# Optimization experiments

Measured on AMD Instinct MI355X. Metric: run time of the kernel, lower is better.

## Reference

```python
import jax, jax.numpy as jnp
import numpy as np

INV_SQRT2 = 0.7071067811865476  # Haar/db1 filter coefficient
LEVEL = 3


def _split(x, axis):
    """One Haar analysis step along `axis` (even length assumed)."""
    ax = axis % x.ndim
    sl0 = [slice(None)] * x.ndim; sl0[ax] = slice(0, None, 2)
    sl1 = [slice(None)] * x.ndim; sl1[ax] = slice(1, None, 2)
    x0, x1 = x[tuple(sl0)], x[tuple(sl1)]
    return (x0 + x1) * INV_SQRT2, (x0 - x1) * INV_SQRT2


def _merge(lo, hi, axis):
    """One Haar synthesis step along `axis` (interleave even/odd)."""
    ax = axis % lo.ndim
    e = (lo + hi) * INV_SQRT2
    o = (lo - hi) * INV_SQRT2
    s = jnp.stack([e, o], axis=ax + 1)
    shape = list(lo.shape)
    shape[ax] *= 2
    return s.reshape(shape)


def _dwt2(x):
    lo, hi = _split(x, -1)
    a, h = _split(lo, -2)
    v, d = _split(hi, -2)
    return a, h, v, d


def _idwt2(a, h, v, d):
    lo = _merge(a, h, -2)
    hi = _merge(v, d, -2)
    return _merge(lo, hi, -1)


def setup_inputs() -> dict:
    key = jax.random.key(0)
    ks = jax.random.split(key, 8)
    B, H, W = 16, 1024, 1024
    x = jax.random.normal(ks[0], (B, H, W, 1), dtype=jnp.float32)
    na = (H // 8) * (W // 8)   # approx size at level 3
    n2 = (H // 4) * (W // 4)
    n1 = (H // 2) * (W // 2)
    scale = 0.02
    Wa = jax.random.normal(ks[1], (na, 1), dtype=jnp.float32) * scale
    ba = jnp.zeros((1,), jnp.float32)
    Wd1 = jax.random.normal(ks[2], (3 * na, 3), dtype=jnp.float32) * scale  # coarsest details
    bd1 = jnp.zeros((3,), jnp.float32)
    Wd2 = jax.random.normal(ks[3], (3 * n2, 3), dtype=jnp.float32) * scale
    bd2 = jnp.zeros((3,), jnp.float32)
    Wd3 = jax.random.normal(ks[4], (3 * n1, 3), dtype=jnp.float32) * scale  # finest details
    bd3 = jnp.zeros((3,), jnp.float32)
    return {"x": x, "Wa": Wa, "ba": ba, "Wd1": Wd1, "bd1": bd1,
            "Wd2": Wd2, "bd2": bd2, "Wd3": Wd3, "bd3": bd3}


def reference(x, Wa, ba, Wd1, bd1, Wd2, bd2, Wd3, bd3):
    img = x[..., 0]                      # [B, H, W]
    B = img.shape[0]
    details = []                         # finest -> coarsest
    cur = img
    for _ in range(LEVEL):
        cur, h, v, d = _dwt2(cur)
        details.append((h, v, d))
    # approximation attention: sigmoid(Dense(1)) scalar gate per sample
    aw = jax.nn.sigmoid(cur.reshape(B, -1) @ Wa + ba)   # [B, 1]
    rec = cur * aw[:, :, None]                           # [B, H/8, W/8]
    # detail attention per level (coarsest first, matching pywt coeff order)
    det_params = [(Wd1, bd1), (Wd2, bd2), (Wd3, bd3)]
    for (h, v, d), (Wd, bd) in zip(reversed(details), det_params):
        flat = jnp.stack([h, v, d], axis=1).reshape(B, -1)      # [B, 3*hl*wl]
        w = jax.nn.softmax(flat @ Wd + bd, axis=-1)             # [B, 3]
        rec = _idwt2(rec,
                     h * w[:, 0, None, None],
                     v * w[:, 1, None, None],
                     d * w[:, 2, None, None])
    return rec                                                   # [B, H, W]
```

## Files before the change

### kernel.cpp

```cpp
#include <hip/hip_runtime.h>
#include <math.h>

#define HH 1024
#define WW 1024
#define N1 262144
#define N2 65536
#define N3 16384
#define BLOCKS_PER_B 64

#define C_INV_SQRT2 0.70710678118654752440f

static __device__ __forceinline__ void haar_fwd(float P, float Q, float R, float S,
                                                float& a, float& h, float& v, float& d) {
    const float C = C_INV_SQRT2;
    float lo0 = (P + Q) * C, lo1 = (R + S) * C;
    float hi0 = (P - Q) * C, hi1 = (R - S) * C;
    a = (lo0 + lo1) * C; h = (lo0 - lo1) * C;
    v = (hi0 + hi1) * C; d = (hi0 - hi1) * C;
}

static __device__ __forceinline__ void haar_inv(float a, float h, float v, float d,
                                                float& P, float& Q, float& R, float& S) {
    const float C = C_INV_SQRT2;
    float elo = (a + h) * C, olo = (a - h) * C;
    float ehi = (v + d) * C, ohi = (v - d) * C;
    P = (elo + ehi) * C; Q = (elo - ehi) * C;
    R = (olo + ohi) * C; S = (olo - ohi) * C;
}

__global__ __launch_bounds__(256) void wa_fwd_dots(
    const float* __restrict__ x,
    const float* __restrict__ Wa,
    const float* __restrict__ Wd1,
    const float* __restrict__ Wd2,
    const float* __restrict__ Wd3,
    float* __restrict__ partial)
{
    const int b = blockIdx.z;
    const int t = threadIdx.x;
    const int tr = t >> 4, tc = t & 15;
    const int y0 = blockIdx.y * 128 + tr * 8;
    const int x0 = blockIdx.x * 128 + tc * 8;

    const float* xb = x + (size_t)b * HH * WW;

    float p[8][8];
    #pragma unroll
    for (int r = 0; r < 8; ++r) {
        const float4* row = (const float4*)(xb + (size_t)(y0 + r) * WW + x0);
        float4 u0 = row[0], u1 = row[1];
        p[r][0] = u0.x; p[r][1] = u0.y; p[r][2] = u0.z; p[r][3] = u0.w;
        p[r][4] = u1.x; p[r][5] = u1.y; p[r][6] = u1.z; p[r][7] = u1.w;
    }

    float acc[10];
    #pragma unroll
    for (int k = 0; k < 10; ++k) acc[k] = 0.f;

    float a1[4][4];
    #pragma unroll
    for (int i = 0; i < 4; ++i) {
        const size_t jj0 = (size_t)((y0 >> 1) + i) * 512 + (size_t)(x0 >> 1);
        float wh[12], wv[12], wd[12];
        {
            const float4* H = (const float4*)(Wd3 + jj0 * 3);
            const float4* V = (const float4*)(Wd3 + (jj0 + (size_t)N1) * 3);
            const float4* D = (const float4*)(Wd3 + (jj0 + (size_t)2 * N1) * 3);
            #pragma unroll
            for (int q = 0; q < 3; ++q) {
                float4 a = H[q]; wh[4*q] = a.x; wh[4*q+1] = a.y; wh[4*q+2] = a.z; wh[4*q+3] = a.w;
                float4 c = V[q]; wv[4*q] = c.x; wv[4*q+1] = c.y; wv[4*q+2] = c.z; wv[4*q+3] = c.w;
                float4 e = D[q]; wd[4*q] = e.x; wd[4*q+1] = e.y; wd[4*q+2] = e.z; wd[4*q+3] = e.w;
            }
        }
        #pragma unroll
        for (int j = 0; j < 4; ++j) {
            float a, h, v, d;
            haar_fwd(p[2*i][2*j], p[2*i][2*j+1], p[2*i+1][2*j], p[2*i+1][2*j+1], a, h, v, d);
            a1[i][j] = a;
            #pragma unroll
            for (int c = 0; c < 3; ++c)
                acc[7 + c] += h * wh[j*3 + c] + v * wv[j*3 + c] + d * wd[j*3 + c];
        }
    }

    float a2[2][2];
    #pragma unroll
    for (int i = 0; i < 2; ++i) {
        const size_t jj0 = (size_t)((y0 >> 2) + i) * 256 + (size_t)(x0 >> 2);
        float wh[6], wv[6], wd[6];
        {
            const float2* H = (const float2*)(Wd2 + jj0 * 3);
            const float2* V = (const float2*)(Wd2 + (jj0 + (size_t)N2) * 3);
            const float2* D = (const float2*)(Wd2 + (jj0 + (size_t)2 * N2) * 3);
            #pragma unroll
            for (int q = 0; q < 3; ++q) {
                float2 a = H[q]; wh[2*q] = a.x; wh[2*q+1] = a.y;
                float2 c = V[q]; wv[2*q] = c.x; wv[2*q+1] = c.y;
                float2 e = D[q]; wd[2*q] = e.x; wd[2*q+1] = e.y;
            }
        }
        #pragma unroll
        for (int j = 0; j < 2; ++j) {
            float a, h, v, d;
            haar_fwd(a1[2*i][2*j], a1[2*i][2*j+1], a1[2*i+1][2*j], a1[2*i+1][2*j+1], a, h, v, d);
            a2[i][j] = a;
            #pragma unroll
            for (int c = 0; c < 3; ++c)
                acc[4 + c] += h * wh[j*3 + c] + v * wv[j*3 + c] + d * wd[j*3 + c];
        }
    }

    {
        float a, h, v, d;
        haar_fwd(a2[0][0], a2[0][1], a2[1][0], a2[1][1], a, h, v, d);
        const size_t jj = (size_t)(y0 >> 3) * 128 + (size_t)(x0 >> 3);
        acc[0] += a * Wa[jj];
        const float* wh = Wd1 + jj * 3;
        const float* wv = Wd1 + (jj + (size_t)N3) * 3;
        const float* wd = Wd1 + (jj + (size_t)2 * N3) * 3;
        #pragma unroll
        for (int c = 0; c < 3; ++c)
            acc[1 + c] += h * wh[c] + v * wv[c] + d * wd[c];
    }

    #pragma unroll
    for (int k = 0; k < 10; ++k) {
        float s = acc[k];
        #pragma unroll
        for (int off = 32; off > 0; off >>= 1) s += __shfl_down(s, off, 64);
        acc[k] = s;
    }
    __shared__ float red[4][10];
    const int lane = t & 63, wave = t >> 6;
    if (lane == 0) {
        #pragma unroll
        for (int k = 0; k < 10; ++k) red[wave][k] = acc[k];
    }
    __syncthreads();
    if (t < 10) {
        const int blkflat = b * BLOCKS_PER_B + blockIdx.y * 8 + blockIdx.x;
        partial[(size_t)blkflat * 10 + t] = red[0][t] + red[1][t] + red[2][t] + red[3][t];
    }
}

__global__ __launch_bounds__(64) void wa_gates(
    const float* __restrict__ partial,
    const float* __restrict__ ba,
    const float* __restrict__ bd1,
    const float* __restrict__ bd2,
    const float* __restrict__ bd3,
    float* __restrict__ gates)
{
    const int b = blockIdx.x;
    const int l = threadIdx.x;
    const float* row = partial + (size_t)(b * BLOCKS_PER_B + l) * 10;
    float v[10];
    #pragma unroll
    for (int k = 0; k < 10; ++k) v[k] = row[k];
    #pragma unroll
    for (int k = 0; k < 10; ++k) {
        #pragma unroll
        for (int off = 32; off > 0; off >>= 1) v[k] += __shfl_down(v[k], off, 64);
    }
    if (l == 0) {
        float* G = gates + b * 10;
        G[0] = 1.f / (1.f + expf(-(v[0] + ba[0])));
        const float* bds[3] = { bd1, bd2, bd3 };
        #pragma unroll
        for (int lv = 0; lv < 3; ++lv) {
            float l0 = v[1 + 3*lv + 0] + bds[lv][0];
            float l1 = v[1 + 3*lv + 1] + bds[lv][1];
            float l2 = v[1 + 3*lv + 2] + bds[lv][2];
            float m = fmaxf(l0, fmaxf(l1, l2));
            float e0 = expf(l0 - m), e1 = expf(l1 - m), e2 = expf(l2 - m);
            float inv = 1.f / (e0 + e1 + e2);
            G[1 + 3*lv + 0] = e0 * inv;
            G[1 + 3*lv + 1] = e1 * inv;
            G[1 + 3*lv + 2] = e2 * inv;
        }
    }
}

__global__ __launch_bounds__(64) void wa_recon(
    const float* __restrict__ x,
    const float* __restrict__ gates,
    float* __restrict__ out)
{
    const int b = blockIdx.z;
    const int t = threadIdx.x;

    __shared__ float g[10];
    if (t < 10) g[t] = gates[b * 10 + t];
    __syncthreads();

    const int tr = t >> 3, tc = t & 7;
    const int y0 = blockIdx.y * 64 + tr * 8;
    const int x0 = blockIdx.x * 64 + tc * 8;

    const float* xb = x + (size_t)b * HH * WW;

    float p[8][8];
    #pragma unroll
    for (int r = 0; r < 8; ++r) {
        const float4* row = (const float4*)(xb + (size_t)(y0 + r) * WW + x0);
        float4 u0 = row[0], u1 = row[1];
        p[r][0] = u0.x; p[r][1] = u0.y; p[r][2] = u0.z; p[r][3] = u0.w;
        p[r][4] = u1.x; p[r][5] = u1.y; p[r][6] = u1.z; p[r][7] = u1.w;
    }

    float a1[4][4], h1[4][4], v1[4][4], d1[4][4];
    #pragma unroll
    for (int i = 0; i < 4; ++i)
        #pragma unroll
        for (int j = 0; j < 4; ++j)
            haar_fwd(p[2*i][2*j], p[2*i][2*j+1], p[2*i+1][2*j], p[2*i+1][2*j+1],
                     a1[i][j], h1[i][j], v1[i][j], d1[i][j]);

    float a2[2][2], h2[2][2], v2[2][2], d2[2][2];
    #pragma unroll
    for (int i = 0; i < 2; ++i)
        #pragma unroll
        for (int j = 0; j < 2; ++j)
            haar_fwd(a1[2*i][2*j], a1[2*i][2*j+1], a1[2*i+1][2*j], a1[2*i+1][2*j+1],
                     a2[i][j], h2[i][j], v2[i][j], d2[i][j]);

    float a3, h3, v3, d3;
    haar_fwd(a2[0][0], a2[0][1], a2[1][0], a2[1][1], a3, h3, v3, d3);

    a3 *= g[0];
    float r2[2][2];
    haar_inv(a3, h3 * g[1], v3 * g[2], d3 * g[3],
             r2[0][0], r2[0][1], r2[1][0], r2[1][1]);

    float r1[4][4];
    #pragma unroll
    for (int i = 0; i < 2; ++i)
        #pragma unroll
        for (int j = 0; j < 2; ++j)
            haar_inv(r2[i][j], h2[i][j] * g[4], v2[i][j] * g[5], d2[i][j] * g[6],
                     r1[2*i][2*j], r1[2*i][2*j+1], r1[2*i+1][2*j], r1[2*i+1][2*j+1]);

    float r0[8][8];
    #pragma unroll
    for (int i = 0; i < 4; ++i)
        #pragma unroll
        for (int j = 0; j < 4; ++j)
            haar_inv(r1[i][j], h1[i][j] * g[7], v1[i][j] * g[8], d1[i][j] * g[9],
                     r0[2*i][2*j], r0[2*i][2*j+1], r0[2*i+1][2*j], r0[2*i+1][2*j+1]);

    float* ob = out + (size_t)b * HH * WW;
    #pragma unroll
    for (int r = 0; r < 8; ++r) {
        float4* row = (float4*)(ob + (size_t)(y0 + r) * WW + x0);
        float4 u0, u1;
        u0.x = r0[r][0]; u0.y = r0[r][1]; u0.z = r0[r][2]; u0.w = r0[r][3];
        u1.x = r0[r][4]; u1.y = r0[r][5]; u1.z = r0[r][6]; u1.w = r0[r][7];
        row[0] = u0; row[1] = u1;
    }
}

extern "C" void kernel_launch(void* const* d_in, const int* in_sizes, int n_in,
                              void* d_out, int out_size, void* d_ws, size_t ws_size,
                              hipStream_t stream) {
    const float* x   = (const float*)d_in[0];
    const float* Wa  = (const float*)d_in[1];
    const float* ba  = (const float*)d_in[2];
    const float* Wd1 = (const float*)d_in[3];
    const float* bd1 = (const float*)d_in[4];
    const float* Wd2 = (const float*)d_in[5];
    const float* bd2 = (const float*)d_in[6];
    const float* Wd3 = (const float*)d_in[7];
    const float* bd3 = (const float*)d_in[8];
    float* out = (float*)d_out;

    const int B = in_sizes[0] / (HH * WW);

    float* partial = (float*)d_ws;
    float* gates   = partial + (size_t)B * BLOCKS_PER_B * 10;

    dim3 fgrid(8, 8, B);
    wa_fwd_dots<<<fgrid, 256, 0, stream>>>(x, Wa, Wd1, Wd2, Wd3, partial);
    wa_gates<<<B, 64, 0, stream>>>(partial, ba, bd1, bd2, bd3, gates);
    dim3 rgrid(16, 16, B);
    wa_recon<<<rgrid, 64, 0, stream>>>(x, gates, out);
}
```

Before: 172.7 us.

## Split 8x8 Haar tiles across four lanes with shuffle exchange for coarser levels

Each thread now loads a 2x8 strip instead of an 8x8 block, and groups of four lanes cooperate on one 8x8 tile, exchanging level-1 and level-2 approximation coefficients via __shfl_xor. Blocks cover 512x8 strips, so each wave reads full contiguous rows for coalescing, and register pressure drops, which allows higher occupancy (launch_bounds 256,8). The gate kernel now sums more per-block partials in a loop. The cost is extra shuffles and select logic, plus some idle lanes at the coarser levels.

```diff
diff --git a/kernel.cpp b/kernel.cpp
--- a/kernel.cpp
+++ b/kernel.cpp
@@ -6,7 +6,8 @@
 #define N1 262144
 #define N2 65536
 #define N3 16384
-#define BLOCKS_PER_B 64
+#define TILE_W 512
+#define BLOCKS_PER_B ((WW / TILE_W) * (HH / 8))
 
 #define C_INV_SQRT2 0.70710678118654752440f
 
@@ -28,7 +29,7 @@
     R = (olo + ohi) * C; S = (olo - ohi) * C;
 }
 
-__global__ __launch_bounds__(256) void wa_fwd_dots(
+__global__ __launch_bounds__(256, 8) void wa_fwd_dots(
     const float* __restrict__ x,
     const float* __restrict__ Wa,
     const float* __restrict__ Wd1,
@@ -38,15 +39,16 @@
 {
     const int b = blockIdx.z;
     const int t = threadIdx.x;
-    const int tr = t >> 4, tc = t & 15;
-    const int y0 = blockIdx.y * 128 + tr * 8;
-    const int x0 = blockIdx.x * 128 + tc * 8;
+    const int k = t >> 2;
+    const int q = t & 3;
+    const int x0 = blockIdx.x * TILE_W + k * 8;
+    const int y0 = blockIdx.y * 8 + q * 2;
 
     const float* xb = x + (size_t)b * HH * WW;
 
-    float p[8][8];
-    #pragma unroll
-    for (int r = 0; r < 8; ++r) {
+    float p[2][8];
+    #pragma unroll
+    for (int r = 0; r < 2; ++r) {
         const float4* row = (const float4*)(xb + (size_t)(y0 + r) * WW + x0);
         float4 u0 = row[0], u1 = row[1];
         p[r][0] = u0.x; p[r][1] = u0.y; p[r][2] = u0.z; p[r][3] = u0.w;
@@ -55,66 +57,84 @@
 
     float acc[10];
     #pragma unroll
-    for (int k = 0; k < 10; ++k) acc[k] = 0.f;
-
-    float a1[4][4];
-    #pragma unroll
-    for (int i = 0; i < 4; ++i) {
-        const size_t jj0 = (size_t)((y0 >> 1) + i) * 512 + (size_t)(x0 >> 1);
-        float wh[12], wv[12], wd[12];
-        {
-            const float4* H = (const float4*)(Wd3 + jj0 * 3);
-            const float4* V = (const float4*)(Wd3 + (jj0 + (size_t)N1) * 3);
-            const float4* D = (const float4*)(Wd3 + (jj0 + (size_t)2 * N1) * 3);
+    for (int c = 0; c < 10; ++c) acc[c] = 0.f;
+
+    float a1[4], hh[4], vv[4], dd[4];
+    #pragma unroll
+    for (int j = 0; j < 4; ++j)
+        haar_fwd(p[0][2*j], p[0][2*j+1], p[1][2*j], p[1][2*j+1],
+                 a1[j], hh[j], vv[j], dd[j]);
+    {
+        const size_t jj0 = (size_t)(blockIdx.y * 4 + q) * 512 + (size_t)(x0 >> 1);
+        const float4* H = (const float4*)(Wd3 + jj0 * 3);
+        const float4* V = (const float4*)(Wd3 + (jj0 + (size_t)N1) * 3);
+        const float4* D = (const float4*)(Wd3 + (jj0 + (size_t)2 * N1) * 3);
+        #pragma unroll
+        for (int s = 0; s < 3; ++s) {
+            const float4* W4 = (s == 0) ? H : (s == 1) ? V : D;
+            const float*  cf = (s == 0) ? hh : (s == 1) ? vv : dd;
+            float w[12];
             #pragma unroll
-            for (int q = 0; q < 3; ++q) {
-                float4 a = H[q]; wh[4*q] = a.x; wh[4*q+1] = a.y; wh[4*q+2] = a.z; wh[4*q+3] = a.w;
-                float4 c = V[q]; wv[4*q] = c.x; wv[4*q+1] = c.y; wv[4*q+2] = c.z; wv[4*q+3] = c.w;
-                float4 e = D[q]; wd[4*q] = e.x; wd[4*q+1] = e.y; wd[4*q+2] = e.z; wd[4*q+3] = e.w;
+            for (int u = 0; u < 3; ++u) {
+                float4 f = W4[u];
+                w[4*u] = f.x; w[4*u+1] = f.y; w[4*u+2] = f.z; w[4*u+3] = f.w;
             }
+            #pragma unroll
+            for (int j = 0; j < 4; ++j)
+                #pragma unroll
+                for (int c = 0; c < 3; ++c)
+                    acc[7 + c] += cf[j] * w[3*j + c];
         }
-        #pragma unroll
-        for (int j = 0; j < 4; ++j) {
-            float a, h, v, d;
-            haar_fwd(p[2*i][2*j], p[2*i][2*j+1], p[2*i+1][2*j], p[2*i+1][2*j+1], a, h, v, d);
-            a1[i][j] = a;
+    }
+
+    float o1[4];
+    #pragma unroll
+    for (int j = 0; j < 4; ++j) o1[j] = __shfl_xor(a1[j], 1);
+    const bool odd = (q & 1);
+    float top[4], bot[4];
+    #pragma unroll
+    for (int j = 0; j < 4; ++j) {
+        top[j] = odd ? o1[j] : a1[j];
+        bot[j] = odd ? a1[j] : o1[j];
+    }
+    float a2[2], h2[2], v2[2], d2[2];
+    #pragma unroll
+    for (int j = 0; j < 2; ++j)
+        haar_fwd(top[2*j], top[2*j+1], bot[2*j], bot[2*j+1],
+                 a2[j], h2[j], v2[j], d2[j]);
+    if (!odd) {
+        const size_t kk0 = (size_t)(blockIdx.y * 2 + (q >> 1)) * 256 + (size_t)(x0 >> 2);
+        const float2* H = (const float2*)(Wd2 + kk0 * 3);
+        const float2* V = (const float2*)(Wd2 + (kk0 + (size_t)N2) * 3);
+        const float2* D = (const float2*)(Wd2 + (kk0 + (size_t)2 * N2) * 3);
+        float wh[6], wv[6], wd[6];
+        #pragma unroll
+        for (int u = 0; u < 3; ++u) {
+            float2 fh = H[u]; wh[2*u] = fh.x; wh[2*u+1] = fh.y;
+            float2 fv = V[u]; wv[2*u] = fv.x; wv[2*u+1] = fv.y;
+            float2 fd = D[u]; wd[2*u] = fd.x; wd[2*u+1] = fd.y;
+        }
+        #pragma unroll
+        for (int j = 0; j < 2; ++j)
             #pragma unroll
             for (int c = 0; c < 3; ++c)
-                acc[7 + c] += h * wh[j*3 + c] + v * wv[j*3 + c] + d * wd[j*3 + c];
-        }
-    }
-
-    float a2[2][2];
-    #pragma unroll
-    for (int i = 0; i < 2; ++i) {
-        const size_t jj0 = (size_t)((y0 >> 2) + i) * 256 + (size_t)(x0 >> 2);
-        float wh[6], wv[6], wd[6];
-        {
-            const float2* H = (const float2*)(Wd2 + jj0 * 3);
-            const float2* V = (const float2*)(Wd2 + (jj0 + (size_t)N2) * 3);
-            const float2* D = (const float2*)(Wd2 + (jj0 + (size_t)2 * N2) * 3);
-            #pragma unroll
-            for (int q = 0; q < 3; ++q) {
-                float2 a = H[q]; wh[2*q] = a.x; wh[2*q+1] = a.y;
-                float2 c = V[q]; wv[2*q] = c.x; wv[2*q+1] = c.y;
-                float2 e = D[q]; wd[2*q] = e.x; wd[2*q+1] = e.y;
-            }
-        }
-        #pragma unroll
-        for (int j = 0; j < 2; ++j) {
-            float a, h, v, d;
-            haar_fwd(a1[2*i][2*j], a1[2*i][2*j+1], a1[2*i+1][2*j], a1[2*i+1][2*j+1], a, h, v, d);
-            a2[i][j] = a;
-            #pragma unroll
-            for (int c = 0; c < 3; ++c)
-                acc[4 + c] += h * wh[j*3 + c] + v * wv[j*3 + c] + d * wd[j*3 + c];
-        }
-    }
-
-    {
+                acc[4 + c] += h2[j] * wh[3*j + c] + v2[j] * wv[3*j + c] + d2[j] * wd[3*j + c];
+    }
+
+    float o2[2];
+    #pragma unroll
+    for (int j = 0; j < 2; ++j) o2[j] = __shfl_xor(a2[j], 2);
+    const bool lower = (q >> 1);
+    float t3[2], b3[2];
+    #pragma unroll
+    for (int j = 0; j < 2; ++j) {
+        t3[j] = lower ? o2[j] : a2[j];
+        b3[j] = lower ? a2[j] : o2[j];
+    }
+    if (q == 0) {
         float a, h, v, d;
-        haar_fwd(a2[0][0], a2[0][1], a2[1][0], a2[1][1], a, h, v, d);
-        const size_t jj = (size_t)(y0 >> 3) * 128 + (size_t)(x0 >> 3);
+        haar_fwd(t3[0], t3[1], b3[0], b3[1], a, h, v, d);
+        const size_t jj = (size_t)blockIdx.y * 128 + (size_t)(x0 >> 3);
         acc[0] += a * Wa[jj];
         const float* wh = Wd1 + jj * 3;
         const float* wv = Wd1 + (jj + (size_t)N3) * 3;
@@ -125,21 +145,21 @@
     }
 
     #pragma unroll
-    for (int k = 0; k < 10; ++k) {
-        float s = acc[k];
+    for (int c = 0; c < 10; ++c) {
+        float s = acc[c];
         #pragma unroll
         for (int off = 32; off > 0; off >>= 1) s += __shfl_down(s, off, 64);
-        acc[k] = s;
+        acc[c] = s;
     }
     __shared__ float red[4][10];
     const int lane = t & 63, wave = t >> 6;
     if (lane == 0) {
         #pragma unroll
-        for (int k = 0; k < 10; ++k) red[wave][k] = acc[k];
+        for (int c = 0; c < 10; ++c) red[wave][c] = acc[c];
     }
     __syncthreads();
     if (t < 10) {
-        const int blkflat = b * BLOCKS_PER_B + blockIdx.y * 8 + blockIdx.x;
+        const int blkflat = b * BLOCKS_PER_B + blockIdx.y * (WW / TILE_W) + blockIdx.x;
         partial[(size_t)blkflat * 10 + t] = red[0][t] + red[1][t] + red[2][t] + red[3][t];
     }
 }
@@ -154,14 +174,19 @@
 {
     const int b = blockIdx.x;
     const int l = threadIdx.x;
-    const float* row = partial + (size_t)(b * BLOCKS_PER_B + l) * 10;
     float v[10];
     #pragma unroll
-    for (int k = 0; k < 10; ++k) v[k] = row[k];
-    #pragma unroll
-    for (int k = 0; k < 10; ++k) {
-        #pragma unroll
-        for (int off = 32; off > 0; off >>= 1) v[k] += __shfl_down(v[k], off, 64);
+    for (int c = 0; c < 10; ++c) v[c] = 0.f;
+    #pragma unroll
+    for (int rep = 0; rep < BLOCKS_PER_B / 64; ++rep) {
+        const float* row = partial + (size_t)(b * BLOCKS_PER_B + rep * 64 + l) * 10;
+        #pragma unroll
+        for (int c = 0; c < 10; ++c) v[c] += row[c];
+    }
+    #pragma unroll
+    for (int c = 0; c < 10; ++c) {
+        #pragma unroll
+        for (int off = 32; off > 0; off >>= 1) v[c] += __shfl_down(v[c], off, 64);
     }
     if (l == 0) {
         float* G = gates + b * 10;
@@ -182,7 +207,7 @@
     }
 }
 
-__global__ __launch_bounds__(64) void wa_recon(
+__global__ __launch_bounds__(256, 8) void wa_recon(
     const float* __restrict__ x,
     const float* __restrict__ gates,
     float* __restrict__ out)
@@ -194,64 +219,85 @@
     if (t < 10) g[t] = gates[b * 10 + t];
     __syncthreads();
 
-    const int tr = t >> 3, tc = t & 7;
-    const int y0 = blockIdx.y * 64 + tr * 8;
-    const int x0 = blockIdx.x * 64 + tc * 8;
+    const int k = t >> 2;
+    const int q = t & 3;
+    const int x0 = blockIdx.x * TILE_W + k * 8;
+    const int y0 = blockIdx.y * 8 + q * 2;
 
     const float* xb = x + (size_t)b * HH * WW;
 
-    float p[8][8];
-    #pragma unroll
-    for (int r = 0; r < 8; ++r) {
+    float p[2][8];
+    #pragma unroll
+    for (int r = 0; r < 2; ++r) {
         const float4* row = (const float4*)(xb + (size_t)(y0 + r) * WW + x0);
         float4 u0 = row[0], u1 = row[1];
         p[r][0] = u0.x; p[r][1] = u0.y; p[r][2] = u0.z; p[r][3] = u0.w;
         p[r][4] = u1.x; p[r][5] = u1.y; p[r][6] = u1.z; p[r][7] = u1.w;
     }
 
-    float a1[4][4], h1[4][4], v1[4][4], d1[4][4];
-    #pragma unroll
-    for (int i = 0; i < 4; ++i)
-        #pragma unroll
-        for (int j = 0; j < 4; ++j)
-            haar_fwd(p[2*i][2*j], p[2*i][2*j+1], p[2*i+1][2*j], p[2*i+1][2*j+1],
-                     a1[i][j], h1[i][j], v1[i][j], d1[i][j]);
-
-    float a2[2][2], h2[2][2], v2[2][2], d2[2][2];
-    #pragma unroll
-    for (int i = 0; i < 2; ++i)
-        #pragma unroll
-        for (int j = 0; j < 2; ++j)
-            haar_fwd(a1[2*i][2*j], a1[2*i][2*j+1], a1[2*i+1][2*j], a1[2*i+1][2*j+1],
-                     a2[i][j], h2[i][j], v2[i][j], d2[i][j]);
-
+    float a1[4], h1[4], v1[4], d1[4];
+    #pragma unroll
+    for (int j = 0; j < 4; ++j)
+        haar_fwd(p[0][2*j], p[0][2*j+1], p[1][2*j], p[1][2*j+1],
+                 a1[j], h1[j], v1[j], d1[j]);
+
+    float o1[4];
+    #pragma unroll
+    for (int j = 0; j < 4; ++j) o1[j] = __shfl_xor(a1[j], 1);
+    const bool odd = (q & 1);
+    float top[4], bot[4];
+    #pragma unroll
+    for (int j = 0; j < 4; ++j) {
+        top[j] = odd ? o1[j] : a1[j];
+        bot[j] = odd ? a1[j] : o1[j];
+    }
+    float a2[2], h2[2], v2[2], d2[2];
+    #pragma unroll
+    for (int j = 0; j < 2; ++j)
+        haar_fwd(top[2*j], top[2*j+1], bot[2*j], bot[2*j+1],
+                 a2[j], h2[j], v2[j], d2[j]);
+
+    float o2[2];
+    #pragma unroll
+    for (int j = 0; j < 2; ++j) o2[j] = __shfl_xor(a2[j], 2);
+    const bool lower = (q >> 1);
+    float t3[2], b3[2];
+    #pragma unroll
+    for (int j = 0; j < 2; ++j) {
+        t3[j] = lower ? o2[j] : a2[j];
+        b3[j] = lower ? a2[j] : o2[j];
+    }
     float a3, h3, v3, d3;
-    haar_fwd(a2[0][0], a2[0][1], a2[1][0], a2[1][1], a3, h3, v3, d3);
+    haar_fwd(t3[0], t3[1], b3[0], b3[1], a3, h3, v3, d3);
 
     a3 *= g[0];
     float r2[2][2];
     haar_inv(a3, h3 * g[1], v3 * g[2], d3 * g[3],
              r2[0][0], r2[0][1], r2[1][0], r2[1][1]);
-
-    float r1[4][4];
-    #pragma unroll
-    for (int i = 0; i < 2; ++i)
-        #pragma unroll
-        for (int j = 0; j < 2; ++j)
-            haar_inv(r2[i][j], h2[i][j] * g[4], v2[i][j] * g[5], d2[i][j] * g[6],
-                     r1[2*i][2*j], r1[2*i][2*j+1], r1[2*i+1][2*j], r1[2*i+1][2*j+1]);
-
-    float r0[8][8];
-    #pragma unroll
-    for (int i = 0; i < 4; ++i)
-        #pragma unroll
-        for (int j = 0; j < 4; ++j)
-            haar_inv(r1[i][j], h1[i][j] * g[7], v1[i][j] * g[8], d1[i][j] * g[9],
-                     r0[2*i][2*j], r0[2*i][2*j+1], r0[2*i+1][2*j], r0[2*i+1][2*j+1]);
+    const int i2 = q >> 1;
+    float r2m0 = r2[i2][0], r2m1 = r2[i2][1];
+
+    float r1[4];
+    {
+        float P, Q, R, S;
+        haar_inv(r2m0, h2[0] * g[4], v2[0] * g[5], d2[0] * g[6], P, Q, R, S);
+        r1[0] = odd ? R : P;  r1[1] = odd ? S : Q;
+        haar_inv(r2m1, h2[1] * g[4], v2[1] * g[5], d2[1] * g[6], P, Q, R, S);
+        r1[2] = odd ? R : P;  r1[3] = odd ? S : Q;
+    }
+
+    float r0[2][8];
+    #pragma unroll
+    for (int j = 0; j < 4; ++j) {
+        float P, Q, R, S;
+        haar_inv(r1[j], h1[j] * g[7], v1[j] * g[8], d1[j] * g[9], P, Q, R, S);
+        r0[0][2*j] = P; r0[0][2*j+1] = Q;
+        r0[1][2*j] = R; r0[1][2*j+1] = S;
+    }
 
     float* ob = out + (size_t)b * HH * WW;
     #pragma unroll
-    for (int r = 0; r < 8; ++r) {
+    for (int r = 0; r < 2; ++r) {
         float4* row = (float4*)(ob + (size_t)(y0 + r) * WW + x0);
         float4 u0, u1;
         u0.x = r0[r][0]; u0.y = r0[r][1]; u0.z = r0[r][2]; u0.w = r0[r][3];
@@ -279,9 +325,8 @@
     float* partial = (float*)d_ws;
     float* gates   = partial + (size_t)B * BLOCKS_PER_B * 10;
 
-    dim3 fgrid(8, 8, B);
-    wa_fwd_dots<<<fgrid, 256, 0, stream>>>(x, Wa, Wd1, Wd2, Wd3, partial);
+    dim3 grid(WW / TILE_W, HH / 8, B);
+    wa_fwd_dots<<<grid, 256, 0, stream>>>(x, Wa, Wd1, Wd2, Wd3, partial);
     wa_gates<<<B, 64, 0, stream>>>(partial, ba, bd1, bd2, bd3, gates);
-    dim3 rgrid(16, 16, B);
-    wa_recon<<<rgrid, 64, 0, stream>>>(x, gates, out);
-}
+    wa_recon<<<grid, 256, 0, stream>>>(x, gates, out);
+}
```

Measured after the change: 182.3 us. +5.6%, slower.

## Restructure DWT kernels into row strips with weights reused across batch images

Applied to the files above, without the earlier changes.

The forward-dot kernel now gives each block an 8-row strip and loops over a chunk of batch images. Each thread loads its weight slices into registers once and reuses them for every image in the chunk, which cuts repeated weight reads from global memory. Each thread now owns a 4-wide column pair, and the level-3 step combines values from neighbouring lanes with shuffles. The reconstruction kernel uses the same strip layout with 256-thread blocks. Per-wave partial sums are written to a larger partial buffer that the gate kernel reduces with a strided loop. The trade-off is more register pressure from the cached weights and fewer blocks in the forward grid.

```diff
diff --git a/kernel.cpp b/kernel.cpp
--- a/kernel.cpp
+++ b/kernel.cpp
@@ -6,7 +6,8 @@
 #define N1 262144
 #define N2 65536
 #define N3 16384
-#define BLOCKS_PER_B 64
+#define NCHUNK 4
+#define ROWS_PER_IMG 512
 
 #define C_INV_SQRT2 0.70710678118654752440f
 
@@ -34,113 +35,110 @@
     const float* __restrict__ Wd1,
     const float* __restrict__ Wd2,
     const float* __restrict__ Wd3,
-    float* __restrict__ partial)
+    float* __restrict__ partial,
+    int ipc)
 {
-    const int b = blockIdx.z;
+    const int strip = blockIdx.x;
+    const int chunk = blockIdx.y;
     const int t = threadIdx.x;
-    const int tr = t >> 4, tc = t & 15;
-    const int y0 = blockIdx.y * 128 + tr * 8;
-    const int x0 = blockIdx.x * 128 + tc * 8;
-
-    const float* xb = x + (size_t)b * HH * WW;
-
-    float p[8][8];
-    #pragma unroll
-    for (int r = 0; r < 8; ++r) {
-        const float4* row = (const float4*)(xb + (size_t)(y0 + r) * WW + x0);
-        float4 u0 = row[0], u1 = row[1];
-        p[r][0] = u0.x; p[r][1] = u0.y; p[r][2] = u0.z; p[r][3] = u0.w;
-        p[r][4] = u1.x; p[r][5] = u1.y; p[r][6] = u1.z; p[r][7] = u1.w;
-    }
-
-    float acc[10];
-    #pragma unroll
-    for (int k = 0; k < 10; ++k) acc[k] = 0.f;
-
-    float a1[4][4];
-    #pragma unroll
-    for (int i = 0; i < 4; ++i) {
-        const size_t jj0 = (size_t)((y0 >> 1) + i) * 512 + (size_t)(x0 >> 1);
-        float wh[12], wv[12], wd[12];
+    const int lane = t & 63, wave = t >> 6;
+
+    float w1[3][4][6];
+    #pragma unroll
+    for (int qr = 0; qr < 4; ++qr) {
+        const size_t jj = (size_t)(strip * 4 + qr) * 512 + 2 * t;
+        #pragma unroll
+        for (int s = 0; s < 3; ++s) {
+            const float2* src = (const float2*)(Wd3 + (jj + (size_t)s * N1) * 3);
+            float2 f0 = src[0], f1 = src[1], f2 = src[2];
+            w1[s][qr][0] = f0.x; w1[s][qr][1] = f0.y; w1[s][qr][2] = f1.x;
+            w1[s][qr][3] = f1.y; w1[s][qr][4] = f2.x; w1[s][qr][5] = f2.y;
+        }
+    }
+    float w2[3][2][3];
+    #pragma unroll
+    for (int QR = 0; QR < 2; ++QR) {
+        const size_t jj = (size_t)(strip * 2 + QR) * 256 + t;
+        #pragma unroll
+        for (int s = 0; s < 3; ++s) {
+            const float* src = Wd2 + (jj + (size_t)s * N2) * 3;
+            w2[s][QR][0] = src[0]; w2[s][QR][1] = src[1]; w2[s][QR][2] = src[2];
+        }
+    }
+    float w3[3][3] = {};
+    float wa = 0.f;
+    if (!(t & 1)) {
+        const size_t jj = (size_t)strip * 128 + (t >> 1);
+        wa = Wa[jj];
+        #pragma unroll
+        for (int s = 0; s < 3; ++s) {
+            const float* src = Wd1 + (jj + (size_t)s * N3) * 3;
+            w3[s][0] = src[0]; w3[s][1] = src[1]; w3[s][2] = src[2];
+        }
+    }
+
+    #pragma unroll 2
+    for (int bi = 0; bi < ipc; ++bi) {
+        const int b = chunk * ipc + bi;
+        const float* xr = x + (size_t)b * HH * WW + (size_t)strip * 8 * WW + 4 * t;
+
+        float acc[10];
+        #pragma unroll
+        for (int c = 0; c < 10; ++c) acc[c] = 0.f;
+
+        float a1[4][2];
+        #pragma unroll
+        for (int qr = 0; qr < 4; ++qr) {
+            float4 u0 = *(const float4*)(xr + (size_t)(2 * qr)     * WW);
+            float4 u1 = *(const float4*)(xr + (size_t)(2 * qr + 1) * WW);
+            float h_[2], v_[2], d_[2];
+            haar_fwd(u0.x, u0.y, u1.x, u1.y, a1[qr][0], h_[0], v_[0], d_[0]);
+            haar_fwd(u0.z, u0.w, u1.z, u1.w, a1[qr][1], h_[1], v_[1], d_[1]);
+            #pragma unroll
+            for (int qc = 0; qc < 2; ++qc)
+                #pragma unroll
+                for (int c = 0; c < 3; ++c)
+                    acc[7 + c] += h_[qc] * w1[0][qr][qc * 3 + c]
+                                + v_[qc] * w1[1][qr][qc * 3 + c]
+                                + d_[qc] * w1[2][qr][qc * 3 + c];
+        }
+
+        float a2[2];
+        #pragma unroll
+        for (int QR = 0; QR < 2; ++QR) {
+            float h2, v2, d2;
+            haar_fwd(a1[2 * QR][0], a1[2 * QR][1], a1[2 * QR + 1][0], a1[2 * QR + 1][1],
+                     a2[QR], h2, v2, d2);
+            #pragma unroll
+            for (int c = 0; c < 3; ++c)
+                acc[4 + c] += h2 * w2[0][QR][c] + v2 * w2[1][QR][c] + d2 * w2[2][QR][c];
+        }
+
         {
-            const float4* H = (const float4*)(Wd3 + jj0 * 3);
-            const float4* V = (const float4*)(Wd3 + (jj0 + (size_t)N1) * 3);
-            const float4* D = (const float4*)(Wd3 + (jj0 + (size_t)2 * N1) * 3);
-            #pragma unroll
-            for (int q = 0; q < 3; ++q) {
-                float4 a = H[q]; wh[4*q] = a.x; wh[4*q+1] = a.y; wh[4*q+2] = a.z; wh[4*q+3] = a.w;
-                float4 c = V[q]; wv[4*q] = c.x; wv[4*q+1] = c.y; wv[4*q+2] = c.z; wv[4*q+3] = c.w;
-                float4 e = D[q]; wd[4*q] = e.x; wd[4*q+1] = e.y; wd[4*q+2] = e.z; wd[4*q+3] = e.w;
+            float oa0 = __shfl_xor(a2[0], 1);
+            float oa1 = __shfl_xor(a2[1], 1);
+            if (!(t & 1)) {
+                float a3, h3, v3, d3;
+                haar_fwd(a2[0], oa0, a2[1], oa1, a3, h3, v3, d3);
+                acc[0] += a3 * wa;
+                #pragma unroll
+                for (int c = 0; c < 3; ++c)
+                    acc[1 + c] += h3 * w3[0][c] + v3 * w3[1][c] + d3 * w3[2][c];
             }
         }
-        #pragma unroll
-        for (int j = 0; j < 4; ++j) {
-            float a, h, v, d;
-            haar_fwd(p[2*i][2*j], p[2*i][2*j+1], p[2*i+1][2*j], p[2*i+1][2*j+1], a, h, v, d);
-            a1[i][j] = a;
-            #pragma unroll
-            for (int c = 0; c < 3; ++c)
-                acc[7 + c] += h * wh[j*3 + c] + v * wv[j*3 + c] + d * wd[j*3 + c];
-        }
-    }
-
-    float a2[2][2];
-    #pragma unroll
-    for (int i = 0; i < 2; ++i) {
-        const size_t jj0 = (size_t)((y0 >> 2) + i) * 256 + (size_t)(x0 >> 2);
-        float wh[6], wv[6], wd[6];
-        {
-            const float2* H = (const float2*)(Wd2 + jj0 * 3);
-            const float2* V = (const float2*)(Wd2 + (jj0 + (size_t)N2) * 3);
-            const float2* D = (const float2*)(Wd2 + (jj0 + (size_t)2 * N2) * 3);
-            #pragma unroll
-            for (int q = 0; q < 3; ++q) {
-                float2 a = H[q]; wh[2*q] = a.x; wh[2*q+1] = a.y;
-                float2 c = V[q]; wv[2*q] = c.x; wv[2*q+1] = c.y;
-                float2 e = D[q]; wd[2*q] = e.x; wd[2*q+1] = e.y;
-            }
-        }
-        #pragma unroll
-        for (int j = 0; j < 2; ++j) {
-            float a, h, v, d;
-            haar_fwd(a1[2*i][2*j], a1[2*i][2*j+1], a1[2*i+1][2*j], a1[2*i+1][2*j+1], a, h, v, d);
-            a2[i][j] = a;
-            #pragma unroll
-            for (int c = 0; c < 3; ++c)
-                acc[4 + c] += h * wh[j*3 + c] + v * wv[j*3 + c] + d * wd[j*3 + c];
-        }
-    }
-
-    {
-        float a, h, v, d;
-        haar_fwd(a2[0][0], a2[0][1], a2[1][0], a2[1][1], a, h, v, d);
-        const size_t jj = (size_t)(y0 >> 3) * 128 + (size_t)(x0 >> 3);
-        acc[0] += a * Wa[jj];
-        const float* wh = Wd1 + jj * 3;
-        const float* wv = Wd1 + (jj + (size_t)N3) * 3;
-        const float* wd = Wd1 + (jj + (size_t)2 * N3) * 3;
-        #pragma unroll
-        for (int c = 0; c < 3; ++c)
-            acc[1 + c] += h * wh[c] + v * wv[c] + d * wd[c];
-    }
-
-    #pragma unroll
-    for (int k = 0; k < 10; ++k) {
-        float s = acc[k];
-        #pragma unroll
-        for (int off = 32; off > 0; off >>= 1) s += __shfl_down(s, off, 64);
-        acc[k] = s;
-    }
-    __shared__ float red[4][10];
-    const int lane = t & 63, wave = t >> 6;
-    if (lane == 0) {
-        #pragma unroll
-        for (int k = 0; k < 10; ++k) red[wave][k] = acc[k];
-    }
-    __syncthreads();
-    if (t < 10) {
-        const int blkflat = b * BLOCKS_PER_B + blockIdx.y * 8 + blockIdx.x;
-        partial[(size_t)blkflat * 10 + t] = red[0][t] + red[1][t] + red[2][t] + red[3][t];
+
+        #pragma unroll
+        for (int c = 0; c < 10; ++c) {
+            float s = acc[c];
+            #pragma unroll
+            for (int off = 1; off < 64; off <<= 1) s += __shfl_xor(s, off);
+            acc[c] = s;
+        }
+        if (lane == 0) {
+            float* row = partial + ((size_t)b * ROWS_PER_IMG + (size_t)strip * 4 + wave) * 10;
+            #pragma unroll
+            for (int c = 0; c < 10; ++c) row[c] = acc[c];
+        }
     }
 }
 
@@ -154,14 +152,18 @@
 {
     const int b = blockIdx.x;
     const int l = threadIdx.x;
-    const float* row = partial + (size_t)(b * BLOCKS_PER_B + l) * 10;
     float v[10];
     #pragma unroll
-    for (int k = 0; k < 10; ++k) v[k] = row[k];
-    #pragma unroll
-    for (int k = 0; k < 10; ++k) {
-        #pragma unroll
-        for (int off = 32; off > 0; off >>= 1) v[k] += __shfl_down(v[k], off, 64);
+    for (int c = 0; c < 10; ++c) v[c] = 0.f;
+    for (int r = l; r < ROWS_PER_IMG; r += 64) {
+        const float* row = partial + ((size_t)b * ROWS_PER_IMG + r) * 10;
+        #pragma unroll
+        for (int c = 0; c < 10; ++c) v[c] += row[c];
+    }
+    #pragma unroll
+    for (int c = 0; c < 10; ++c) {
+        #pragma unroll
+        for (int off = 1; off < 64; off <<= 1) v[c] += __shfl_xor(v[c], off);
     }
     if (l == 0) {
         float* G = gates + b * 10;
@@ -169,94 +171,80 @@
         const float* bds[3] = { bd1, bd2, bd3 };
         #pragma unroll
         for (int lv = 0; lv < 3; ++lv) {
-            float l0 = v[1 + 3*lv + 0] + bds[lv][0];
-            float l1 = v[1 + 3*lv + 1] + bds[lv][1];
-            float l2 = v[1 + 3*lv + 2] + bds[lv][2];
+            float l0 = v[1 + 3 * lv + 0] + bds[lv][0];
+            float l1 = v[1 + 3 * lv + 1] + bds[lv][1];
+            float l2 = v[1 + 3 * lv + 2] + bds[lv][2];
             float m = fmaxf(l0, fmaxf(l1, l2));
             float e0 = expf(l0 - m), e1 = expf(l1 - m), e2 = expf(l2 - m);
             float inv = 1.f / (e0 + e1 + e2);
-            G[1 + 3*lv + 0] = e0 * inv;
-            G[1 + 3*lv + 1] = e1 * inv;
-            G[1 + 3*lv + 2] = e2 * inv;
-        }
-    }
-}
-
-__global__ __launch_bounds__(64) void wa_recon(
+            G[1 + 3 * lv + 0] = e0 * inv;
+            G[1 + 3 * lv + 1] = e1 * inv;
+            G[1 + 3 * lv + 2] = e2 * inv;
+        }
+    }
+}
+
+__global__ __launch_bounds__(256) void wa_recon(
     const float* __restrict__ x,
     const float* __restrict__ gates,
     float* __restrict__ out)
 {
-    const int b = blockIdx.z;
+    const int strip = blockIdx.x;
+    const int b = blockIdx.y;
     const int t = threadIdx.x;
 
     __shared__ float g[10];
     if (t < 10) g[t] = gates[b * 10 + t];
     __syncthreads();
 
-    const int tr = t >> 3, tc = t & 7;
-    const int y0 = blockIdx.y * 64 + tr * 8;
-    const int x0 = blockIdx.x * 64 + tc * 8;
-
-    const float* xb = x + (size_t)b * HH * WW;
-
-    float p[8][8];
-    #pragma unroll
-    for (int r = 0; r < 8; ++r) {
-        const float4* row = (const float4*)(xb + (size_t)(y0 + r) * WW + x0);
-        float4 u0 = row[0], u1 = row[1];
-        p[r][0] = u0.x; p[r][1] = u0.y; p[r][2] = u0.z; p[r][3] = u0.w;
-        p[r][4] = u1.x; p[r][5] = u1.y; p[r][6] = u1.z; p[r][7] = u1.w;
-    }
-
-    float a1[4][4], h1[4][4], v1[4][4], d1[4][4];
-    #pragma unroll
-    for (int i = 0; i < 4; ++i)
-        #pragma unroll
-        for (int j = 0; j < 4; ++j)
-            haar_fwd(p[2*i][2*j], p[2*i][2*j+1], p[2*i+1][2*j], p[2*i+1][2*j+1],
-                     a1[i][j], h1[i][j], v1[i][j], d1[i][j]);
-
-    float a2[2][2], h2[2][2], v2[2][2], d2[2][2];
-    #pragma unroll
-    for (int i = 0; i < 2; ++i)
-        #pragma unroll
-        for (int j = 0; j < 2; ++j)
-            haar_fwd(a1[2*i][2*j], a1[2*i][2*j+1], a1[2*i+1][2*j], a1[2*i+1][2*j+1],
-                     a2[i][j], h2[i][j], v2[i][j], d2[i][j]);
-
+    const float* xr = x + (size_t)b * HH * WW + (size_t)strip * 8 * WW + 4 * t;
+
+    float a1[4][2], h1[4][2], v1[4][2], d1[4][2];
+    #pragma unroll
+    for (int qr = 0; qr < 4; ++qr) {
+        float4 u0 = *(const float4*)(xr + (size_t)(2 * qr)     * WW);
+        float4 u1 = *(const float4*)(xr + (size_t)(2 * qr + 1) * WW);
+        haar_fwd(u0.x, u0.y, u1.x, u1.y, a1[qr][0], h1[qr][0], v1[qr][0], d1[qr][0]);
+        haar_fwd(u0.z, u0.w, u1.z, u1.w, a1[qr][1], h1[qr][1], v1[qr][1], d1[qr][1]);
+    }
+    float a2[2], h2[2], v2[2], d2[2];
+    #pragma unroll
+    for (int QR = 0; QR < 2; ++QR)
+        haar_fwd(a1[2 * QR][0], a1[2 * QR][1], a1[2 * QR + 1][0], a1[2 * QR + 1][1],
+                 a2[QR], h2[QR], v2[QR], d2[QR]);
+
+    float oa0 = __shfl_xor(a2[0], 1);
+    float oa1 = __shfl_xor(a2[1], 1);
+    const bool rightside = t & 1;
     float a3, h3, v3, d3;
-    haar_fwd(a2[0][0], a2[0][1], a2[1][0], a2[1][1], a3, h3, v3, d3);
+    if (!rightside) haar_fwd(a2[0], oa0, a2[1], oa1, a3, h3, v3, d3);
+    else            haar_fwd(oa0, a2[0], oa1, a2[1], a3, h3, v3, d3);
 
     a3 *= g[0];
-    float r2[2][2];
-    haar_inv(a3, h3 * g[1], v3 * g[2], d3 * g[3],
-             r2[0][0], r2[0][1], r2[1][0], r2[1][1]);
-
-    float r1[4][4];
-    #pragma unroll
-    for (int i = 0; i < 2; ++i)
-        #pragma unroll
-        for (int j = 0; j < 2; ++j)
-            haar_inv(r2[i][j], h2[i][j] * g[4], v2[i][j] * g[5], d2[i][j] * g[6],
-                     r1[2*i][2*j], r1[2*i][2*j+1], r1[2*i+1][2*j], r1[2*i+1][2*j+1]);
-
-    float r0[8][8];
-    #pragma unroll
-    for (int i = 0; i < 4; ++i)
-        #pragma unroll
-        for (int j = 0; j < 4; ++j)
-            haar_inv(r1[i][j], h1[i][j] * g[7], v1[i][j] * g[8], d1[i][j] * g[9],
-                     r0[2*i][2*j], r0[2*i][2*j+1], r0[2*i+1][2*j], r0[2*i+1][2*j+1]);
-
-    float* ob = out + (size_t)b * HH * WW;
-    #pragma unroll
-    for (int r = 0; r < 8; ++r) {
-        float4* row = (float4*)(ob + (size_t)(y0 + r) * WW + x0);
-        float4 u0, u1;
-        u0.x = r0[r][0]; u0.y = r0[r][1]; u0.z = r0[r][2]; u0.w = r0[r][3];
-        u1.x = r0[r][4]; u1.y = r0[r][5]; u1.z = r0[r][6]; u1.w = r0[r][7];
-        row[0] = u0; row[1] = u1;
+    float P, Q, R, S;
+    haar_inv(a3, h3 * g[1], v3 * g[2], d3 * g[3], P, Q, R, S);
+    float r2[2];
+    r2[0] = rightside ? Q : P;
+    r2[1] = rightside ? S : R;
+
+    float ra1[4][2];
+    #pragma unroll
+    for (int QR = 0; QR < 2; ++QR) {
+        haar_inv(r2[QR], h2[QR] * g[4], v2[QR] * g[5], d2[QR] * g[6], P, Q, R, S);
+        ra1[2 * QR][0] = P; ra1[2 * QR][1] = Q;
+        ra1[2 * QR + 1][0] = R; ra1[2 * QR + 1][1] = S;
+    }
+
+    float* orow = out + (size_t)b * HH * WW + (size_t)strip * 8 * WW + 4 * t;
+    #pragma unroll
+    for (int qr = 0; qr < 4; ++qr) {
+        float4 o0, o1;
+        haar_inv(ra1[qr][0], h1[qr][0] * g[7], v1[qr][0] * g[8], d1[qr][0] * g[9],
+                 o0.x, o0.y, o1.x, o1.y);
+        haar_inv(ra1[qr][1], h1[qr][1] * g[7], v1[qr][1] * g[8], d1[qr][1] * g[9],
+                 o0.z, o0.w, o1.z, o1.w);
+        *(float4*)(orow + (size_t)(2 * qr)     * WW) = o0;
+        *(float4*)(orow + (size_t)(2 * qr + 1) * WW) = o1;
     }
 }
 
@@ -277,11 +265,14 @@
     const int B = in_sizes[0] / (HH * WW);
 
     float* partial = (float*)d_ws;
-    float* gates   = partial + (size_t)B * BLOCKS_PER_B * 10;
-
-    dim3 fgrid(8, 8, B);
-    wa_fwd_dots<<<fgrid, 256, 0, stream>>>(x, Wa, Wd1, Wd2, Wd3, partial);
+    float* gates   = partial + (size_t)B * ROWS_PER_IMG * 10;
+
+    int nchunk = NCHUNK, ipc = B / NCHUNK;
+    if (B % NCHUNK) { nchunk = B; ipc = 1; }
+
+    dim3 fgrid(128, nchunk);
+    wa_fwd_dots<<<fgrid, 256, 0, stream>>>(x, Wa, Wd1, Wd2, Wd3, partial, ipc);
     wa_gates<<<B, 64, 0, stream>>>(partial, ba, bd1, bd2, bd3, gates);
-    dim3 rgrid(16, 16, B);
-    wa_recon<<<rgrid, 64, 0, stream>>>(x, gates, out);
-}
+    dim3 rgrid(128, B);
+    wa_recon<<<rgrid, 256, 0, stream>>>(x, gates, out);
+}
```

Result: faster. 155.7 us (-9.9%).
